# Kernel optimization log

Measured on AMD Instinct MI355X. Metric: run time of the kernel, lower is better.

## Reference

```python
import jax, jax.numpy as jnp
import numpy as np

B, N, D = 32, 512, 1024
H, DH = 8, 64
INNER = H * DH          # 512
PROJ = 512
MID = (D + PROJ) // 2   # 768
EPS = 1e-5


def _ln(x, gamma):
    # F.layer_norm over last dim, beta is a zeros buffer
    m = jnp.mean(x, axis=-1, keepdims=True)
    v = jnp.var(x, axis=-1, keepdims=True)
    return (x - m) * jax.lax.rsqrt(v + EPS) * gamma


def setup_inputs() -> dict:
    key = jax.random.key(0)
    ks = jax.random.split(key, 12)
    s = 0.02
    return {
        "x": jax.random.normal(ks[0], (B, N, D), dtype=jnp.float32),
        "pos_encoding": jax.random.normal(ks[1], (1, N, D), dtype=jnp.float32),
        "queries": jax.random.normal(ks[2], (N, D), dtype=jnp.float32),
        "ln_q_g": jnp.ones((D,), dtype=jnp.float32),
        "ln_ctx_g": jnp.ones((D,), dtype=jnp.float32),
        "Wq": jax.random.normal(ks[3], (D, INNER), dtype=jnp.float32) * s,
        "Wkv": jax.random.normal(ks[4], (D, 2 * DH), dtype=jnp.float32) * s,
        "Wout": jax.random.normal(ks[5], (INNER, D), dtype=jnp.float32) * s,
        "ln_post_g": jnp.ones((D,), dtype=jnp.float32),
        "W1": jax.random.normal(ks[6], (D, MID), dtype=jnp.float32) * s,
        "b1": jnp.zeros((MID,), dtype=jnp.float32),
        "W2": jax.random.normal(ks[7], (MID, PROJ), dtype=jnp.float32) * s,
        "b2": jnp.zeros((PROJ,), dtype=jnp.float32),
        "zero_masks": jnp.ones((B, N), dtype=jnp.int32),  # unused (masking commented out in source)
    }


def reference(x, pos_encoding, queries, ln_q_g, ln_ctx_g, Wq, Wkv, Wout,
              ln_post_g, W1, b1, W2, b2, zero_masks):
    scale = DH ** -0.5
    x = x.astype(jnp.float32) + pos_encoding                   # [B,N,D]
    q_in = jnp.broadcast_to(queries[None], (B, N, D))          # learned queries per batch

    # CrossAttention (norm_context=True, parallel_ff=False)
    qn = _ln(q_in, ln_q_g)
    ctx = _ln(x, ln_ctx_g)
    q = (qn @ Wq).reshape(B, N, H, DH).transpose(0, 2, 1, 3) * scale   # [B,H,N,DH]
    kv = ctx @ Wkv                                                     # [B,N,2*DH]
    k, v = kv[..., :DH], kv[..., DH:]                                  # shared across heads (MQA)
    sim = jnp.einsum('bhid,bjd->bhij', q, k)                           # [B,H,N,N]
    attn = jax.nn.softmax(sim, axis=-1)                                # max-subtract stable
    out = jnp.einsum('bhij,bjd->bhid', attn, v)                        # [B,H,N,DH]
    out = out.transpose(0, 2, 1, 3).reshape(B, N, INNER) @ Wout        # [B,N,D]

    out = _ln(out, ln_post_g)
    emb = jnp.mean(out, axis=1)                                        # [B,D] video embedding
    pred = jax.nn.gelu(emb @ W1 + b1, approximate=False) @ W2 + b2     # [B,PROJ]
    return pred
```

## Files before the change

### kernel.cpp

```cpp
#include <hip/hip_runtime.h>
#include <cmath>

#define Bz 32
#define Nz 512
#define Dz 1024
#define Hz 8
#define DHz 64
#define INNERz 512
#define PROJz 512
#define MIDz 768
#define EPSz 1e-5f

typedef unsigned short u16;
typedef unsigned int u32;
typedef __attribute__((ext_vector_type(8))) short short8v;
typedef __attribute__((ext_vector_type(8))) unsigned short ushort8v;
typedef __attribute__((ext_vector_type(4))) unsigned short ushort4v;
typedef __attribute__((ext_vector_type(4))) float f32x4;

__device__ __forceinline__ u16 f2bf(float x) {
  unsigned u = __float_as_uint(x);
  unsigned r = u + 0x7fff + ((u >> 16) & 1);
  return (u16)(r >> 16);
}
__device__ __forceinline__ float bf2f(u16 u) {
  return __uint_as_float(((unsigned)u) << 16);
}
__device__ __forceinline__ float fexp2(float x) {
  float r;
  asm("v_exp_f32 %0, %1" : "=v"(r) : "v"(x));
  return r;
}
__device__ __forceinline__ u32 cvtpk(float lo, float hi) {
  u32 r;
  asm("v_cvt_pk_bf16_f32 %0, %1, %2" : "=v"(r) : "v"(lo), "v"(hi));
  return r;
}

__global__ __launch_bounds__(256) void k_prepw(
    const float* __restrict__ Wkv, const float* __restrict__ Wq,
    const float* __restrict__ g_ctx, const float* __restrict__ g_q,
    u16* __restrict__ WkvTg, u16* __restrict__ WqTg,
    float* __restrict__ cskv4, float* __restrict__ csq4) {
  __shared__ float part[64][4];
  const int t = threadIdx.x;
  const int blk = blockIdx.x;
  const int jg = blk >> 2, quarter = blk & 3;
  const bool isq = jg >= 2;
  const int jbase = isq ? (jg - 2) * 64 : jg * 64;
  const int j = jbase + (t & 63);
  const int dsub = t >> 6;
  const float* W = isq ? Wq : Wkv;
  const int ld = isq ? 512 : 128;
  const float* g = isq ? g_q : g_ctx;
  const float scale = isq ? 0.125f * 1.4426950408889634f : 1.f;
  u16* WT = isq ? WqTg : WkvTg;
  float partial = 0.f;
  const int d0beg = quarter * 256 + dsub * 64;
  for (int d0 = d0beg; d0 < d0beg + 64; d0 += 2) {
    const float v0 = scale * g[d0] * W[(size_t)d0 * ld + j];
    const float v1 = scale * g[d0 + 1] * W[(size_t)(d0 + 1) * ld + j];
    partial += v0 + v1;
    *(u32*)(WT + (size_t)j * Dz + d0) = (u32)f2bf(v0) | ((u32)f2bf(v1) << 16);
  }
  part[t & 63][dsub] = partial;
  __syncthreads();
  if (t < 64)
    (isq ? csq4 : cskv4)[(jbase + t) * 4 + quarter] =
        part[t][0] + part[t][1] + part[t][2] + part[t][3];
}

#define LOADB2(dst, kk)                                                        \
  {                                                                            \
    _Pragma("unroll") for (int u_ = 0; u_ < 4; ++u_)                           \
    _Pragma("unroll") for (int cf_ = 0; cf_ < 2; ++cf_)                        \
        dst[u_][cf_] =                                                         \
            *(const short8v*)(Bp + (size_t)cf_ * 16 * Dz + (kk) + u_ * 32);    \
  }

__global__ __launch_bounds__(256) void k_qproj(
    const float* __restrict__ queries, const u16* __restrict__ WT,
    const float* __restrict__ cs4, u16* __restrict__ qbuf) {
  __shared__ u16 hbuf[16 * 1024];
  __shared__ float mm[16], rr[16];
  char* hb = (char*)hbuf;
  const int t = threadIdx.x;
  const int w = t >> 6, l = t & 63;
  const int lr = l & 15, lk = l >> 4;
  const int c0 = blockIdx.y * 128 + w * 32;
  const u16* Bp = WT + (size_t)(c0 + lr) * Dz + lk * 8;
  short8v bcur[4][2], bnxt[4][2];
  LOADB2(bcur, 0);
  {
    const int r = t >> 4, c16 = t & 15;
    const long grow = (long)blockIdx.x * 16 + r;
    const float* xr = queries + grow * Dz;
    float s = 0.f, ss = 0.f;
    const int swz = (r & 7) << 4;
#pragma unroll
    for (int i = 0; i < 16; ++i) {
      const int col = c16 * 4 + i * 64;
      const float4 v = *(const float4*)(xr + col);
      s += (v.x + v.y) + (v.z + v.w);
      ss += (v.x * v.x + v.y * v.y) + (v.z * v.z + v.w * v.w);
      uint2 pk;
      pk.x = (u32)f2bf(v.x) | ((u32)f2bf(v.y) << 16);
      pk.y = (u32)f2bf(v.z) | ((u32)f2bf(v.w) << 16);
      *(uint2*)(hb + ((r * 2048 + col * 2) ^ swz)) = pk;
    }
#pragma unroll
    for (int off = 1; off <= 8; off <<= 1) { s += __shfl_xor(s, off); ss += __shfl_xor(ss, off); }
    const float mean = s * (1.f / Dz);
    const float rstd = rsqrtf(ss * (1.f / Dz) - mean * mean + EPSz);
    if (c16 == 0) { mm[r] = mean; rr[r] = rstd; }
  }
  __syncthreads();
  f32x4 acc[2];
  acc[0] = {0.f, 0.f, 0.f, 0.f};
  acc[1] = {0.f, 0.f, 0.f, 0.f};
  const int aswz = (lr & 7) << 4;
#pragma unroll
  for (int k0 = 0; k0 < Dz; k0 += 128) {
    if (k0 + 128 < Dz) LOADB2(bnxt, k0 + 128);
#pragma unroll
    for (int u = 0; u < 4; ++u) {
      const int kk = (k0 + u * 32 + lk * 8) * 2;
      const short8v a = *(const short8v*)(hb + ((lr * 2048 + kk) ^ aswz));
      acc[0] = __builtin_amdgcn_mfma_f32_16x16x32_bf16(a, bcur[u][0], acc[0], 0, 0, 0);
      acc[1] = __builtin_amdgcn_mfma_f32_16x16x32_bf16(a, bcur[u][1], acc[1], 0, 0, 0);
    }
    if (k0 + 128 < Dz) {
#pragma unroll
      for (int u = 0; u < 4; ++u) {
        bcur[u][0] = bnxt[u][0];
        bcur[u][1] = bnxt[u][1];
      }
    }
  }
  const long base = (long)blockIdx.x * 16;
#pragma unroll
  for (int cf = 0; cf < 2; ++cf) {
    const int col = c0 + cf * 16 + lr;
    const float c = cs4[col * 4] + cs4[col * 4 + 1] + cs4[col * 4 + 2] + cs4[col * 4 + 3];
#pragma unroll
    for (int q = 0; q < 4; ++q) {
      const int row = lk * 4 + q;
      qbuf[(size_t)(base + row) * INNERz + col] = f2bf(rr[row] * (acc[cf][q] - mm[row] * c));
    }
  }
}

__global__ __launch_bounds__(256) void k_ctxkv(
    const float* __restrict__ x, const float* __restrict__ pos,
    const u16* __restrict__ WT, const float* __restrict__ cs4,
    u16* __restrict__ kb, u16* __restrict__ vT) {
  __shared__ u16 hbuf[32 * 1024];
  __shared__ float mm[32], rrs[32];
  char* hb = (char*)hbuf;
  const int t = threadIdx.x;
  const int w = t >> 6, l = t & 63;
  const int lr = l & 15, lk = l >> 4;
  const int c0 = w * 32;
  const u16* Bp = WT + (size_t)(c0 + lr) * Dz + lk * 8;
  short8v bcur[4][2], bnxt[4][2];
  LOADB2(bcur, 0);
  {
    const int r2 = t >> 4, c16 = t & 15;
#pragma unroll
    for (int half = 0; half < 2; ++half) {
      const int r = r2 + half * 16;
      const long grow = (long)blockIdx.x * 32 + r;
      const int n = (int)(grow & (Nz - 1));
      const float* xr = x + grow * Dz;
      const float* pr = pos + (size_t)n * Dz;
      float s = 0.f, ss = 0.f;
      const int swz = (r & 7) << 4;
#pragma unroll
      for (int i = 0; i < 16; ++i) {
        const int col = c16 * 4 + i * 64;
        float4 v = *(const float4*)(xr + col);
        const float4 p = *(const float4*)(pr + col);
        v.x += p.x; v.y += p.y; v.z += p.z; v.w += p.w;
        s += (v.x + v.y) + (v.z + v.w);
        ss += (v.x * v.x + v.y * v.y) + (v.z * v.z + v.w * v.w);
        uint2 pk;
        pk.x = (u32)f2bf(v.x) | ((u32)f2bf(v.y) << 16);
        pk.y = (u32)f2bf(v.z) | ((u32)f2bf(v.w) << 16);
        *(uint2*)(hb + ((r * 2048 + col * 2) ^ swz)) = pk;
      }
#pragma unroll
      for (int off = 1; off <= 8; off <<= 1) { s += __shfl_xor(s, off); ss += __shfl_xor(ss, off); }
      const float mean = s * (1.f / Dz);
      const float rstd = rsqrtf(ss * (1.f / Dz) - mean * mean + EPSz);
      if (c16 == 0) { mm[r] = mean; rrs[r] = rstd; }
    }
  }
  __syncthreads();
  f32x4 acc[2][2];
#pragma unroll
  for (int rf = 0; rf < 2; ++rf)
#pragma unroll
    for (int cf = 0; cf < 2; ++cf) acc[rf][cf] = {0.f, 0.f, 0.f, 0.f};
  const int aswz = (lr & 7) << 4;
#pragma unroll
  for (int k0 = 0; k0 < Dz; k0 += 128) {
    if (k0 + 128 < Dz) LOADB2(bnxt, k0 + 128);
#pragma unroll
    for (int u = 0; u < 4; ++u) {
      const int kk = (k0 + u * 32 + lk * 8) * 2;
      const short8v a0 = *(const short8v*)(hb + ((lr * 2048 + kk) ^ aswz));
      const short8v a1 = *(const short8v*)(hb + (((lr + 16) * 2048 + kk) ^ aswz));
      acc[0][0] = __builtin_amdgcn_mfma_f32_16x16x32_bf16(a0, bcur[u][0], acc[0][0], 0, 0, 0);
      acc[0][1] = __builtin_amdgcn_mfma_f32_16x16x32_bf16(a0, bcur[u][1], acc[0][1], 0, 0, 0);
      acc[1][0] = __builtin_amdgcn_mfma_f32_16x16x32_bf16(a1, bcur[u][0], acc[1][0], 0, 0, 0);
      acc[1][1] = __builtin_amdgcn_mfma_f32_16x16x32_bf16(a1, bcur[u][1], acc[1][1], 0, 0, 0);
    }
    if (k0 + 128 < Dz) {
#pragma unroll
      for (int u = 0; u < 4; ++u) {
        bcur[u][0] = bnxt[u][0];
        bcur[u][1] = bnxt[u][1];
      }
    }
  }
  const long base = (long)blockIdx.x * 32;
  const int bb = (int)(base >> 9), nb0 = (int)(base & (Nz - 1));
#pragma unroll
  for (int rf = 0; rf < 2; ++rf)
#pragma unroll
    for (int cf = 0; cf < 2; ++cf) {
      const int col = c0 + cf * 16 + lr;
      const float c = cs4[col * 4] + cs4[col * 4 + 1] + cs4[col * 4 + 2] + cs4[col * 4 + 3];
      if (col < 64) {
#pragma unroll
        for (int q = 0; q < 4; ++q) {
          const int row = rf * 16 + lk * 4 + q;
          kb[(size_t)(base + row) * DHz + col] = f2bf(rrs[row] * (acc[rf][cf][q] - mm[row] * c));
        }
      } else {
        ushort4v pk;
#pragma unroll
        for (int q = 0; q < 4; ++q) {
          const int row = rf * 16 + lk * 4 + q;
          pk[q] = f2bf(rrs[row] * (acc[rf][cf][q] - mm[row] * c));
        }
        *(ushort4v*)(vT + ((size_t)bb * DHz + (col - 64)) * Nz + nb0 + rf * 16 + lk * 4) = pk;
      }
    }
}

__global__ __launch_bounds__(256) void k_attn(
    const u16* __restrict__ qb, const u16* __restrict__ kb,
    const u16* __restrict__ vT, u16* __restrict__ ao) {
  __shared__ u16 Ks[2][4096];
  __shared__ u16 Vs[2][4096];
  __shared__ u16 plds[4][1024];
  const int t = threadIdx.x;
  const int w = t >> 6, l = t & 63;
  const int lr = l & 15, lk = l >> 4;
  const int m0 = blockIdx.x * 64 + w * 16;
  const int h = blockIdx.y, b = blockIdx.z;
  const u16* qrow = qb + (size_t)(m0 + lr) * INNERz + h * DHz + lk * 8;
  const short8v aq0 = *(const short8v*)qrow;
  const short8v aq1 = *(const short8v*)(qrow + 32);
  const u16* kbB = kb + (size_t)b * Nz * DHz;
  const u16* vTB = vT + (size_t)b * DHz * Nz;
  char* pw = (char*)&plds[w][0];
  const int swz = (lr & 7) << 4;

  const int srow = w * 16 + (l >> 3);
  const int schunk = (l & 7) ^ (l >> 3);

#define STAGE(bufi, j0v)                                                              \
  {                                                                                   \
    _Pragma("unroll") for (int c = 0; c < 2; ++c) {                                   \
      __builtin_amdgcn_global_load_lds(                                               \
          (const __attribute__((address_space(1))) u32*)(const void*)(                \
              kbB + (size_t)((j0v) + srow + c * 8) * DHz + schunk * 8),               \
          (__attribute__((address_space(3))) u32*)(void*)(&Ks[bufi][0] + w * 1024 + c * 512), \
          16, 0, 0);                                                                  \
      __builtin_amdgcn_global_load_lds(                                               \
          (const __attribute__((address_space(1))) u32*)(const void*)(                \
              vTB + (size_t)(srow + c * 8) * Nz + (j0v) + schunk * 8),                \
          (__attribute__((address_space(3))) u32*)(void*)(&Vs[bufi][0] + w * 1024 + c * 512), \
          16, 0, 0);                                                                  \
    }                                                                                 \
  }

  f32x4 oacc[4];
#pragma unroll
  for (int dn = 0; dn < 4; ++dn) oacc[dn] = {0.f, 0.f, 0.f, 0.f};
  float lsum = 0.f;

  int buf = 0;
  STAGE(0, 0);
  asm volatile("s_waitcnt vmcnt(0)" ::: "memory");
  __builtin_amdgcn_s_barrier();
  asm volatile("" ::: "memory");

  for (int tt = 0; tt < 8; ++tt) {
    if (tt < 7) STAGE(buf ^ 1, (tt + 1) * 64);
    asm volatile("" ::: "memory");
    const char* Kb = (const char*)&Ks[buf][0];
    const char* Vb = (const char*)&Vs[buf][0];
    f32x4 sfr[4];
#pragma unroll
    for (int jn = 0; jn < 4; ++jn) {
      const int rbase = jn * 2048 + lr * 128;
      const short8v bk0 = *(const short8v*)(Kb + rbase + ((lk * 16) ^ swz));
      const short8v bk1 = *(const short8v*)(Kb + rbase + ((64 + lk * 16) ^ swz));
      f32x4 c = {0.f, 0.f, 0.f, 0.f};
      c = __builtin_amdgcn_mfma_f32_16x16x32_bf16(bk0, aq0, c, 0, 0, 0);
      c = __builtin_amdgcn_mfma_f32_16x16x32_bf16(bk1, aq1, c, 0, 0, 0);
      sfr[jn] = c;
    }
    float ps = 0.f;
#pragma unroll
    for (int jn = 0; jn < 4; ++jn) {
      const float e0 = fexp2(sfr[jn][0]);
      const float e1 = fexp2(sfr[jn][1]);
      const float e2 = fexp2(sfr[jn][2]);
      const float e3 = fexp2(sfr[jn][3]);
      ps += (e0 + e1) + (e2 + e3);
      const u32 p01 = cvtpk(e0, e1);
      const u32 p23 = cvtpk(e2, e3);
      const int pbase = (lr * 128 + jn * 32 + lk * 8) ^ swz;
      *(u32*)(pw + pbase) = p01;
      *(u32*)(pw + pbase + 4) = p23;
    }
    lsum += ps;
    const short8v pa0 = *(const short8v*)(pw + ((lr * 128 + lk * 16) ^ swz));
    const short8v pa1 = *(const short8v*)(pw + ((lr * 128 + 64 + lk * 16) ^ swz));
#pragma unroll
    for (int dn = 0; dn < 4; ++dn) {
      const int rbase = dn * 2048 + lr * 128;
      const short8v bv0 = *(const short8v*)(Vb + rbase + ((lk * 16) ^ swz));
      const short8v bv1 = *(const short8v*)(Vb + rbase + ((64 + lk * 16) ^ swz));
      f32x4 o = oacc[dn];
      o = __builtin_amdgcn_mfma_f32_16x16x32_bf16(pa0, bv0, o, 0, 0, 0);
      o = __builtin_amdgcn_mfma_f32_16x16x32_bf16(pa1, bv1, o, 0, 0, 0);
      oacc[dn] = o;
    }
    asm volatile("" ::: "memory");
    if (tt < 7) asm volatile("s_waitcnt vmcnt(0)" ::: "memory");
    __builtin_amdgcn_s_barrier();
    asm volatile("" ::: "memory");
    buf ^= 1;
  }
#undef STAGE
  lsum += __shfl_xor(lsum, 16);
  lsum += __shfl_xor(lsum, 32);
  float rinv[4];
#pragma unroll
  for (int r = 0; r < 4; ++r) rinv[r] = 1.f / __shfl(lsum, lk * 4 + r, 64);
#pragma unroll
  for (int dn = 0; dn < 4; ++dn)
#pragma unroll
    for (int r = 0; r < 4; ++r) {
      const int row = m0 + lk * 4 + r;
      ao[((size_t)b * Nz + row) * INNERz + h * DHz + dn * 16 + lr] =
          f2bf(oacc[dn][r] * rinv[r]);
    }
}

__global__ __launch_bounds__(256) void k_prep(const float* __restrict__ Wout,
                                              u16* __restrict__ WoutT) {
  __shared__ float sm[32][33];
  const int t = threadIdx.x;
  const int n0 = blockIdx.x * 32, k0 = blockIdx.y * 32;
  {
    const int kk = t >> 3, nn = (t & 7) * 4;
    const float4 v = *reinterpret_cast<const float4*>(Wout + (size_t)(k0 + kk) * Dz + n0 + nn);
    sm[kk][nn] = v.x; sm[kk][nn + 1] = v.y; sm[kk][nn + 2] = v.z; sm[kk][nn + 3] = v.w;
  }
  __syncthreads();
  const int nn = t >> 3, kk = (t & 7) * 4;
  ushort4v pk;
#pragma unroll
  for (int j = 0; j < 4; ++j) pk[j] = f2bf(sm[kk + j][nn]);
  *reinterpret_cast<ushort4v*>(WoutT + (size_t)(n0 + nn) * INNERz + k0 + kk) = pk;
}

__global__ __launch_bounds__(256) void k_wgemm(
    const u16* __restrict__ A, const u16* __restrict__ BT, u16* __restrict__ C) {
  __shared__ u16 As[128 * 64];
  __shared__ u16 Bs[128 * 64];
  const int t = threadIdx.x;
  const int w = t >> 6, l = t & 63;
  const int m0 = blockIdx.y * 128, n0 = blockIdx.x * 128;
  const int wr = w >> 1, wc = w & 1;
  const int lr = l & 15, lk = l >> 4;

  f32x4 acc[4][4];
#pragma unroll
  for (int mt = 0; mt < 4; ++mt)
#pragma unroll
    for (int nt = 0; nt < 4; ++nt) acc[mt][nt] = {0.f, 0.f, 0.f, 0.f};

  for (int k0 = 0; k0 < INNERz; k0 += 64) {
#pragma unroll
    for (int c = 0; c < 4; ++c) {
      const int rowblk = w * 32 + c * 8;
      const int row = rowblk + (l >> 3);
      const int kb16 = (l & 7) * 8;
      __builtin_amdgcn_global_load_lds(
          (const __attribute__((address_space(1))) unsigned int*)(const void*)(
              A + (size_t)(m0 + row) * INNERz + k0 + kb16),
          (__attribute__((address_space(3))) unsigned int*)(void*)(As + rowblk * 64),
          16, 0, 0);
      __builtin_amdgcn_global_load_lds(
          (const __attribute__((address_space(1))) unsigned int*)(const void*)(
              BT + (size_t)(n0 + row) * INNERz + k0 + kb16),
          (__attribute__((address_space(3))) unsigned int*)(void*)(Bs + rowblk * 64),
          16, 0, 0);
    }
    __syncthreads();
#pragma unroll
    for (int ks = 0; ks < 2; ++ks) {
      short8v af[4], bf[4];
#pragma unroll
      for (int mt = 0; mt < 4; ++mt)
        af[mt] = *reinterpret_cast<const short8v*>(As + (wr * 64 + mt * 16 + lr) * 64 + ks * 32 + lk * 8);
#pragma unroll
      for (int nt = 0; nt < 4; ++nt)
        bf[nt] = *reinterpret_cast<const short8v*>(Bs + (wc * 64 + nt * 16 + lr) * 64 + ks * 32 + lk * 8);
#pragma unroll
      for (int mt = 0; mt < 4; ++mt)
#pragma unroll
        for (int nt = 0; nt < 4; ++nt)
          acc[mt][nt] = __builtin_amdgcn_mfma_f32_16x16x32_bf16(af[mt], bf[nt], acc[mt][nt], 0, 0, 0);
    }
    __syncthreads();
  }
#pragma unroll
  for (int mt = 0; mt < 4; ++mt)
#pragma unroll
    for (int nt = 0; nt < 4; ++nt) {
      const f32x4 a = acc[mt][nt];
#pragma unroll
      for (int r = 0; r < 4; ++r) {
        const size_t row = (size_t)m0 + wr * 64 + mt * 16 + lk * 4 + r;
        C[row * Dz + n0 + wc * 64 + nt * 16 + lr] = f2bf(a[r]);
      }
    }
}

__global__ __launch_bounds__(256) void k_lnmean(
    const u16* __restrict__ out1, float* __restrict__ pbuf) {
  const int t = threadIdx.x;
  const int w = t >> 6, l = t & 63;
  const long row0 = (long)blockIdx.x * 64 + w * 16;
  float acc[16];
#pragma unroll
  for (int j = 0; j < 16; ++j) acc[j] = 0.f;
  for (int rr = 0; rr < 16; ++rr) {
    const u16* rowp = out1 + (size_t)(row0 + rr) * Dz + l * 16;
    const ushort8v u0 = *(const ushort8v*)(rowp);
    const ushort8v u1 = *(const ushort8v*)(rowp + 8);
    float v[16];
#pragma unroll
    for (int j = 0; j < 8; ++j) { v[j] = bf2f(u0[j]); v[8 + j] = bf2f(u1[j]); }
    float s = 0.f, q = 0.f;
#pragma unroll
    for (int j = 0; j < 16; ++j) { s += v[j]; q += v[j] * v[j]; }
#pragma unroll
    for (int off = 1; off <= 32; off <<= 1) { s += __shfl_xor(s, off); q += __shfl_xor(q, off); }
    const float mean = s * (1.f / Dz);
    const float rstd = rsqrtf(q * (1.f / Dz) - mean * mean + EPSz);
#pragma unroll
    for (int j = 0; j < 16; ++j) acc[j] += (v[j] - mean) * rstd;
  }
  float* dst = pbuf + ((size_t)blockIdx.x * 4 + w) * Dz + l * 16;
#pragma unroll
  for (int j = 0; j < 4; ++j)
    *(float4*)(dst + j * 4) =
        make_float4(acc[j * 4], acc[j * 4 + 1], acc[j * 4 + 2], acc[j * 4 + 3]);
}

__global__ __launch_bounds__(256) void k_embred(
    const float* __restrict__ pbuf, const float* __restrict__ g,
    float* __restrict__ emb) {
  const int b = blockIdx.x, t = threadIdx.x;
  const float invN = 1.f / (float)Nz;
  const float* src = pbuf + (size_t)b * 32 * Dz + t * 4;
  float4 s = {0.f, 0.f, 0.f, 0.f};
#pragma unroll 8
  for (int sub = 0; sub < 32; ++sub) {
    const float4 v = *(const float4*)(src + (size_t)sub * Dz);
    s.x += v.x; s.y += v.y; s.z += v.z; s.w += v.w;
  }
  const float4 gv = *(const float4*)(g + t * 4);
  float4 o;
  o.x = s.x * gv.x * invN;
  o.y = s.y * gv.y * invN;
  o.z = s.z * gv.z * invN;
  o.w = s.w * gv.w * invN;
  *(float4*)(emb + (size_t)b * Dz + t * 4) = o;
}

__global__ __launch_bounds__(256) void k_mlp1(
    const float* __restrict__ emb, const float* __restrict__ W1,
    const float* __restrict__ b1, float* __restrict__ mid) {
  __shared__ float e[Dz];
  __shared__ float red[4][64];
  const int b = blockIdx.y, t = threadIdx.x;
  const int col0 = blockIdx.x * 64;
  *reinterpret_cast<float4*>(&e[t * 4]) =
      *reinterpret_cast<const float4*>(emb + (size_t)b * Dz + t * 4);
  __syncthreads();
  const int q = t >> 6, j = t & 63;
  float acc = 0.f;
  const float* W = W1 + (size_t)(q * 256) * MIDz + col0 + j;
#pragma unroll 8
  for (int k = 0; k < 256; ++k) acc += e[q * 256 + k] * W[(size_t)k * MIDz];
  red[q][j] = acc;
  __syncthreads();
  if (t < 64) {
    const float s = red[0][t] + red[1][t] + red[2][t] + red[3][t] + b1[col0 + t];
    mid[(size_t)b * MIDz + col0 + t] = 0.5f * s * (1.f + erff(s * 0.7071067811865475f));
  }
}

__global__ __launch_bounds__(256) void k_mlp2(
    const float* __restrict__ mid, const float* __restrict__ W2,
    const float* __restrict__ b2, float* __restrict__ out) {
  __shared__ float e[MIDz];
  __shared__ float red[4][64];
  const int b = blockIdx.y, t = threadIdx.x;
  const int col0 = blockIdx.x * 64;
  if (t < MIDz / 4)
    *reinterpret_cast<float4*>(&e[t * 4]) =
        *reinterpret_cast<const float4*>(mid + (size_t)b * MIDz + t * 4);
  __syncthreads();
  const int q = t >> 6, j = t & 63;
  float acc = 0.f;
  const float* W = W2 + (size_t)(q * 192) * PROJz + col0 + j;
#pragma unroll 8
  for (int k = 0; k < 192; ++k) acc += e[q * 192 + k] * W[(size_t)k * PROJz];
  red[q][j] = acc;
  __syncthreads();
  if (t < 64)
    out[(size_t)b * PROJz + col0 + t] =
        red[0][t] + red[1][t] + red[2][t] + red[3][t] + b2[col0 + t];
}

extern "C" void kernel_launch(void* const* d_in, const int* in_sizes, int n_in,
                              void* d_out, int out_size, void* d_ws, size_t ws_size,
                              hipStream_t stream) {
  const float* x         = (const float*)d_in[0];
  const float* pos       = (const float*)d_in[1];
  const float* queries   = (const float*)d_in[2];
  const float* ln_q_g    = (const float*)d_in[3];
  const float* ln_ctx_g  = (const float*)d_in[4];
  const float* Wq        = (const float*)d_in[5];
  const float* Wkv       = (const float*)d_in[6];
  const float* Wout      = (const float*)d_in[7];
  const float* ln_post_g = (const float*)d_in[8];
  const float* W1        = (const float*)d_in[9];
  const float* b1        = (const float*)d_in[10];
  const float* W2        = (const float*)d_in[11];
  const float* b2        = (const float*)d_in[12];
  float* out = (float*)d_out;

  char* wsb = (char*)d_ws;
  float* emb   = (float*)wsb;
  float* mid   = (float*)(wsb + 131072);
  u16*   WoutT = (u16*)(wsb + 229376);
  u16*   aobf  = (u16*)(wsb + 1277952);
  float* pbuf  = (float*)(wsb + 1277952);
  u16*   out1  = (u16*)(wsb + 18055168);
  u16*   WkvTg = (u16*)(wsb + 18055168);
  u16*   WqTg  = (u16*)(wsb + 18317312);
  float* cskv4 = (float*)(wsb + 19365888);
  float* csq4  = (float*)(wsb + 19367936);
  u16*   qbbf  = (u16*)(wsb + 19376128);
  u16*   kbbf  = (u16*)(wsb + 19900416);
  u16*   vTbf  = (u16*)(wsb + 21997568);

  k_prepw<<<40, 256, 0, stream>>>(Wkv, Wq, ln_ctx_g, ln_q_g, WkvTg, WqTg, cskv4, csq4);
  k_prep<<<dim3(Dz / 32, INNERz / 32), 256, 0, stream>>>(Wout, WoutT);
  k_qproj<<<dim3(Nz / 16, 4), 256, 0, stream>>>(queries, WqTg, csq4, qbbf);
  k_ctxkv<<<(Bz * Nz) / 32, 256, 0, stream>>>(x, pos, WkvTg, cskv4, kbbf, vTbf);
  k_attn<<<dim3(Nz / 64, Hz, Bz), 256, 0, stream>>>(qbbf, kbbf, vTbf, aobf);
  k_wgemm<<<dim3(Dz / 128, (Bz * Nz) / 128), 256, 0, stream>>>(aobf, WoutT, out1);
  k_lnmean<<<(Bz * Nz) / 64, 256, 0, stream>>>(out1, pbuf);
  k_embred<<<Bz, 256, 0, stream>>>(pbuf, ln_post_g, emb);
  k_mlp1<<<dim3(MIDz / 64, Bz), 256, 0, stream>>>(emb, W1, b1, mid);
  k_mlp2<<<dim3(PROJz / 64, Bz), 256, 0, stream>>>(mid, W2, b2, out);
}
```

Measured before the change: 158.8 us.

## Process two heads per attention block, fuse Wout prep, swizzle wgemm blocks

The attention kernel now handles two heads per block. Each staged K/V tile in shared memory is reused for both heads, which halves K/V global traffic and the number of blocks. The Wout transpose kernel is folded into k_prepw as extra blocks to save one launch. The output GEMM remaps block indices so that consecutive blocks share tiles and get better L2 reuse. In exchange, attention uses more registers and more LDS for the P buffers, which may reduce occupancy.

```diff
diff --git a/kernel.cpp b/kernel.cpp
--- a/kernel.cpp
+++ b/kernel.cpp
@@ -41,10 +41,28 @@
     const float* __restrict__ Wkv, const float* __restrict__ Wq,
     const float* __restrict__ g_ctx, const float* __restrict__ g_q,
     u16* __restrict__ WkvTg, u16* __restrict__ WqTg,
-    float* __restrict__ cskv4, float* __restrict__ csq4) {
+    float* __restrict__ cskv4, float* __restrict__ csq4,
+    const float* __restrict__ Wout, u16* __restrict__ WoutT) {
   __shared__ float part[64][4];
+  __shared__ float sm[32][33];
   const int t = threadIdx.x;
   const int blk = blockIdx.x;
+  if (blk >= 40) {
+    const int bid2 = blk - 40;
+    const int n0 = (bid2 & 31) * 32, k0 = (bid2 >> 5) * 32;
+    {
+      const int kk = t >> 3, nn = (t & 7) * 4;
+      const float4 v = *reinterpret_cast<const float4*>(Wout + (size_t)(k0 + kk) * Dz + n0 + nn);
+      sm[kk][nn] = v.x; sm[kk][nn + 1] = v.y; sm[kk][nn + 2] = v.z; sm[kk][nn + 3] = v.w;
+    }
+    __syncthreads();
+    const int nn = t >> 3, kk = (t & 7) * 4;
+    ushort4v pk;
+#pragma unroll
+    for (int j = 0; j < 4; ++j) pk[j] = f2bf(sm[kk + j][nn]);
+    *reinterpret_cast<ushort4v*>(WoutT + (size_t)(n0 + nn) * INNERz + k0 + kk) = pk;
+    return;
+  }
   const int jg = blk >> 2, quarter = blk & 3;
   const bool isq = jg >= 2;
   const int jbase = isq ? (jg - 2) * 64 : jg * 64;
@@ -254,18 +272,22 @@
     const u16* __restrict__ vT, u16* __restrict__ ao) {
   __shared__ u16 Ks[2][4096];
   __shared__ u16 Vs[2][4096];
-  __shared__ u16 plds[4][1024];
+  __shared__ u16 plds[4][2048];
   const int t = threadIdx.x;
   const int w = t >> 6, l = t & 63;
   const int lr = l & 15, lk = l >> 4;
   const int m0 = blockIdx.x * 64 + w * 16;
-  const int h = blockIdx.y, b = blockIdx.z;
-  const u16* qrow = qb + (size_t)(m0 + lr) * INNERz + h * DHz + lk * 8;
-  const short8v aq0 = *(const short8v*)qrow;
-  const short8v aq1 = *(const short8v*)(qrow + 32);
+  const int h0 = blockIdx.y * 2;
+  const int b = blockIdx.z;
+  const u16* qr = qb + (size_t)(m0 + lr) * INNERz + h0 * DHz + lk * 8;
+  const short8v aq00 = *(const short8v*)qr;
+  const short8v aq01 = *(const short8v*)(qr + 32);
+  const short8v aq10 = *(const short8v*)(qr + 64);
+  const short8v aq11 = *(const short8v*)(qr + 96);
   const u16* kbB = kb + (size_t)b * Nz * DHz;
   const u16* vTB = vT + (size_t)b * DHz * Nz;
-  char* pw = (char*)&plds[w][0];
+  char* pw0 = (char*)&plds[w][0];
+  char* pw1 = (char*)&plds[w][1024];
   const int swz = (lr & 7) << 4;
 
   const int srow = w * 16 + (l >> 3);
@@ -287,10 +309,10 @@
     }                                                                                 \
   }
 
-  f32x4 oacc[4];
-#pragma unroll
-  for (int dn = 0; dn < 4; ++dn) oacc[dn] = {0.f, 0.f, 0.f, 0.f};
-  float lsum = 0.f;
+  f32x4 oacc0[4], oacc1[4];
+#pragma unroll
+  for (int dn = 0; dn < 4; ++dn) { oacc0[dn] = {0.f, 0.f, 0.f, 0.f}; oacc1[dn] = {0.f, 0.f, 0.f, 0.f}; }
+  float lsum0 = 0.f, lsum1 = 0.f;
 
   int buf = 0;
   STAGE(0, 0);
@@ -303,43 +325,75 @@
     asm volatile("" ::: "memory");
     const char* Kb = (const char*)&Ks[buf][0];
     const char* Vb = (const char*)&Vs[buf][0];
-    f32x4 sfr[4];
-#pragma unroll
-    for (int jn = 0; jn < 4; ++jn) {
-      const int rbase = jn * 2048 + lr * 128;
-      const short8v bk0 = *(const short8v*)(Kb + rbase + ((lk * 16) ^ swz));
-      const short8v bk1 = *(const short8v*)(Kb + rbase + ((64 + lk * 16) ^ swz));
-      f32x4 c = {0.f, 0.f, 0.f, 0.f};
-      c = __builtin_amdgcn_mfma_f32_16x16x32_bf16(bk0, aq0, c, 0, 0, 0);
-      c = __builtin_amdgcn_mfma_f32_16x16x32_bf16(bk1, aq1, c, 0, 0, 0);
-      sfr[jn] = c;
-    }
-    float ps = 0.f;
-#pragma unroll
-    for (int jn = 0; jn < 4; ++jn) {
-      const float e0 = fexp2(sfr[jn][0]);
-      const float e1 = fexp2(sfr[jn][1]);
-      const float e2 = fexp2(sfr[jn][2]);
-      const float e3 = fexp2(sfr[jn][3]);
-      ps += (e0 + e1) + (e2 + e3);
-      const u32 p01 = cvtpk(e0, e1);
-      const u32 p23 = cvtpk(e2, e3);
-      const int pbase = (lr * 128 + jn * 32 + lk * 8) ^ swz;
-      *(u32*)(pw + pbase) = p01;
-      *(u32*)(pw + pbase + 4) = p23;
-    }
-    lsum += ps;
-    const short8v pa0 = *(const short8v*)(pw + ((lr * 128 + lk * 16) ^ swz));
-    const short8v pa1 = *(const short8v*)(pw + ((lr * 128 + 64 + lk * 16) ^ swz));
+    {
+      f32x4 sfr[4];
+#pragma unroll
+      for (int jn = 0; jn < 4; ++jn) {
+        const int rbase = jn * 2048 + lr * 128;
+        const short8v bk0 = *(const short8v*)(Kb + rbase + ((lk * 16) ^ swz));
+        const short8v bk1 = *(const short8v*)(Kb + rbase + ((64 + lk * 16) ^ swz));
+        f32x4 c = {0.f, 0.f, 0.f, 0.f};
+        c = __builtin_amdgcn_mfma_f32_16x16x32_bf16(bk0, aq00, c, 0, 0, 0);
+        c = __builtin_amdgcn_mfma_f32_16x16x32_bf16(bk1, aq01, c, 0, 0, 0);
+        sfr[jn] = c;
+      }
+      float ps = 0.f;
+#pragma unroll
+      for (int jn = 0; jn < 4; ++jn) {
+        const float e0 = fexp2(sfr[jn][0]);
+        const float e1 = fexp2(sfr[jn][1]);
+        const float e2 = fexp2(sfr[jn][2]);
+        const float e3 = fexp2(sfr[jn][3]);
+        ps += (e0 + e1) + (e2 + e3);
+        const int pbase = (lr * 128 + jn * 32 + lk * 8) ^ swz;
+        *(u32*)(pw0 + pbase) = cvtpk(e0, e1);
+        *(u32*)(pw0 + pbase + 4) = cvtpk(e2, e3);
+      }
+      lsum0 += ps;
+    }
+    {
+      f32x4 sfr[4];
+#pragma unroll
+      for (int jn = 0; jn < 4; ++jn) {
+        const int rbase = jn * 2048 + lr * 128;
+        const short8v bk0 = *(const short8v*)(Kb + rbase + ((lk * 16) ^ swz));
+        const short8v bk1 = *(const short8v*)(Kb + rbase + ((64 + lk * 16) ^ swz));
+        f32x4 c = {0.f, 0.f, 0.f, 0.f};
+        c = __builtin_amdgcn_mfma_f32_16x16x32_bf16(bk0, aq10, c, 0, 0, 0);
+        c = __builtin_amdgcn_mfma_f32_16x16x32_bf16(bk1, aq11, c, 0, 0, 0);
+        sfr[jn] = c;
+      }
+      float ps = 0.f;
+#pragma unroll
+      for (int jn = 0; jn < 4; ++jn) {
+        const float e0 = fexp2(sfr[jn][0]);
+        const float e1 = fexp2(sfr[jn][1]);
+        const float e2 = fexp2(sfr[jn][2]);
+        const float e3 = fexp2(sfr[jn][3]);
+        ps += (e0 + e1) + (e2 + e3);
+        const int pbase = (lr * 128 + jn * 32 + lk * 8) ^ swz;
+        *(u32*)(pw1 + pbase) = cvtpk(e0, e1);
+        *(u32*)(pw1 + pbase + 4) = cvtpk(e2, e3);
+      }
+      lsum1 += ps;
+    }
+    const short8v pa00 = *(const short8v*)(pw0 + ((lr * 128 + lk * 16) ^ swz));
+    const short8v pa01 = *(const short8v*)(pw0 + ((lr * 128 + 64 + lk * 16) ^ swz));
+    const short8v pa10 = *(const short8v*)(pw1 + ((lr * 128 + lk * 16) ^ swz));
+    const short8v pa11 = *(const short8v*)(pw1 + ((lr * 128 + 64 + lk * 16) ^ swz));
 #pragma unroll
     for (int dn = 0; dn < 4; ++dn) {
       const int rbase = dn * 2048 + lr * 128;
       const short8v bv0 = *(const short8v*)(Vb + rbase + ((lk * 16) ^ swz));
       const short8v bv1 = *(const short8v*)(Vb + rbase + ((64 + lk * 16) ^ swz));
-      f32x4 o = oacc[dn];
-      o = __builtin_amdgcn_mfma_f32_16x16x32_bf16(pa0, bv0, o, 0, 0, 0);
-      o = __builtin_amdgcn_mfma_f32_16x16x32_bf16(pa1, bv1, o, 0, 0, 0);
-      oacc[dn] = o;
+      f32x4 o0 = oacc0[dn];
+      o0 = __builtin_amdgcn_mfma_f32_16x16x32_bf16(pa00, bv0, o0, 0, 0, 0);
+      o0 = __builtin_amdgcn_mfma_f32_16x16x32_bf16(pa01, bv1, o0, 0, 0, 0);
+      oacc0[dn] = o0;
+      f32x4 o1 = oacc1[dn];
+      o1 = __builtin_amdgcn_mfma_f32_16x16x32_bf16(pa10, bv0, o1, 0, 0, 0);
+      o1 = __builtin_amdgcn_mfma_f32_16x16x32_bf16(pa11, bv1, o1, 0, 0, 0);
+      oacc1[dn] = o1;
     }
     asm volatile("" ::: "memory");
     if (tt < 7) asm volatile("s_waitcnt vmcnt(0)" ::: "memory");
@@ -348,37 +402,25 @@
     buf ^= 1;
   }
 #undef STAGE
-  lsum += __shfl_xor(lsum, 16);
-  lsum += __shfl_xor(lsum, 32);
-  float rinv[4];
-#pragma unroll
-  for (int r = 0; r < 4; ++r) rinv[r] = 1.f / __shfl(lsum, lk * 4 + r, 64);
+  lsum0 += __shfl_xor(lsum0, 16);
+  lsum0 += __shfl_xor(lsum0, 32);
+  lsum1 += __shfl_xor(lsum1, 16);
+  lsum1 += __shfl_xor(lsum1, 32);
+  float rinv0[4], rinv1[4];
+#pragma unroll
+  for (int r = 0; r < 4; ++r) {
+    rinv0[r] = 1.f / __shfl(lsum0, lk * 4 + r, 64);
+    rinv1[r] = 1.f / __shfl(lsum1, lk * 4 + r, 64);
+  }
 #pragma unroll
   for (int dn = 0; dn < 4; ++dn)
 #pragma unroll
     for (int r = 0; r < 4; ++r) {
       const int row = m0 + lk * 4 + r;
-      ao[((size_t)b * Nz + row) * INNERz + h * DHz + dn * 16 + lr] =
-          f2bf(oacc[dn][r] * rinv[r]);
-    }
-}
-
-__global__ __launch_bounds__(256) void k_prep(const float* __restrict__ Wout,
-                                              u16* __restrict__ WoutT) {
-  __shared__ float sm[32][33];
-  const int t = threadIdx.x;
-  const int n0 = blockIdx.x * 32, k0 = blockIdx.y * 32;
-  {
-    const int kk = t >> 3, nn = (t & 7) * 4;
-    const float4 v = *reinterpret_cast<const float4*>(Wout + (size_t)(k0 + kk) * Dz + n0 + nn);
-    sm[kk][nn] = v.x; sm[kk][nn + 1] = v.y; sm[kk][nn + 2] = v.z; sm[kk][nn + 3] = v.w;
-  }
-  __syncthreads();
-  const int nn = t >> 3, kk = (t & 7) * 4;
-  ushort4v pk;
-#pragma unroll
-  for (int j = 0; j < 4; ++j) pk[j] = f2bf(sm[kk + j][nn]);
-  *reinterpret_cast<ushort4v*>(WoutT + (size_t)(n0 + nn) * INNERz + k0 + kk) = pk;
+      const size_t rbase = ((size_t)b * Nz + row) * INNERz;
+      ao[rbase + h0 * DHz + dn * 16 + lr] = f2bf(oacc0[dn][r] * rinv0[r]);
+      ao[rbase + (h0 + 1) * DHz + dn * 16 + lr] = f2bf(oacc1[dn][r] * rinv1[r]);
+    }
 }
 
 __global__ __launch_bounds__(256) void k_wgemm(
@@ -387,7 +429,9 @@
   __shared__ u16 Bs[128 * 64];
   const int t = threadIdx.x;
   const int w = t >> 6, l = t & 63;
-  const int m0 = blockIdx.y * 128, n0 = blockIdx.x * 128;
+  const int lin = blockIdx.y * gridDim.x + blockIdx.x;
+  const int swzl = (lin & 7) * 128 + (lin >> 3);
+  const int m0 = (swzl >> 3) * 128, n0 = (swzl & 7) * 128;
   const int wr = w >> 1, wc = w & 1;
   const int lr = l & 15, lk = l >> 4;
 
@@ -577,11 +621,11 @@
   u16*   kbbf  = (u16*)(wsb + 19900416);
   u16*   vTbf  = (u16*)(wsb + 21997568);
 
-  k_prepw<<<40, 256, 0, stream>>>(Wkv, Wq, ln_ctx_g, ln_q_g, WkvTg, WqTg, cskv4, csq4);
-  k_prep<<<dim3(Dz / 32, INNERz / 32), 256, 0, stream>>>(Wout, WoutT);
+  k_prepw<<<552, 256, 0, stream>>>(Wkv, Wq, ln_ctx_g, ln_q_g, WkvTg, WqTg, cskv4, csq4,
+                                   Wout, WoutT);
   k_qproj<<<dim3(Nz / 16, 4), 256, 0, stream>>>(queries, WqTg, csq4, qbbf);
   k_ctxkv<<<(Bz * Nz) / 32, 256, 0, stream>>>(x, pos, WkvTg, cskv4, kbbf, vTbf);
-  k_attn<<<dim3(Nz / 64, Hz, Bz), 256, 0, stream>>>(qbbf, kbbf, vTbf, aobf);
+  k_attn<<<dim3(Nz / 64, Hz / 2, Bz), 256, 0, stream>>>(qbbf, kbbf, vTbf, aobf);
   k_wgemm<<<dim3(Dz / 128, (Bz * Nz) / 128), 256, 0, stream>>>(aobf, WoutT, out1);
   k_lnmean<<<(Bz * Nz) / 64, 256, 0, stream>>>(out1, pbuf);
   k_embred<<<Bz, 256, 0, stream>>>(pbuf, ln_post_g, emb);
```

Result: no change. 157.5 us (-0.8%).
